# Optimization experiments

Hardware: AMD Instinct MI355X
Metric: run time of the kernel (lower is better)

The kernel has to match this reference:

```python
import jax, jax.numpy as jnp
import numpy as np

EPS = 1e-12  # torch F.normalize eps


def _l2norm(x):
    n = jnp.linalg.norm(x, axis=-1, keepdims=True)
    return x / jnp.maximum(n, EPS)


def setup_inputs() -> dict:
    key = jax.random.key(0)
    k1, k2 = jax.random.split(key)
    B, Lq, Lk, D = 128, 32, 128, 128
    left_emb = jax.random.normal(k1, (B, Lq, D), dtype=jnp.float32)
    right_emb = jax.random.normal(k2, (B, Lk, D), dtype=jnp.float32)
    pos_idx = jnp.arange(B, dtype=jnp.int64)
    logit_scale = jnp.asarray(np.log(1.0 / 0.07), dtype=jnp.float32)  # scalar param
    return {"left_emb": left_emb, "right_emb": right_emb,
            "logit_scale": logit_scale, "pos_idx": pos_idx}


def reference(left_emb, right_emb, logit_scale, pos_idx):
    # maxsim_colbert: normalize token embeddings, cross-sim, max over doc
    # tokens, sum over query tokens -> [B, B] logits, then CE loss.
    l = _l2norm(left_emb)   # [B, Lq, D]
    r = _l2norm(right_emb)  # [B, Lk, D]
    sims = jnp.einsum('xik,yjk->xyij', l, r)        # [B, B, Lq, Lk]
    sim = sims.max(axis=-1).sum(axis=-1)            # [B, B]
    logits = jnp.exp(logit_scale) * sim
    logp = jax.nn.log_softmax(logits, axis=1)
    B = logits.shape[0]
    loss = -jnp.mean(logp[jnp.arange(B), pos_idx])
    return loss
```

## Files before the change

kernel.cpp:

```cpp
#include <hip/hip_runtime.h>
#include <hip/hip_bf16.h>

typedef short bf16x8 __attribute__((ext_vector_type(8)));
typedef float f32x4 __attribute__((ext_vector_type(4)));
typedef unsigned short u16;

#define B 128
#define LQ 32
#define LK 128
#define D 128
#define YPB 4
#define TILE_BYTES 32768


static __device__ inline u16 f2bf_rne(float f) {
  union { float f; unsigned u; } v; v.f = f;
  unsigned r = v.u + 0x7fffu + ((v.u >> 16) & 1u);
  return (u16)(r >> 16);
}

__global__ __launch_bounds__(256) void normalize_kernel(
    const float* __restrict__ left, const float* __restrict__ right,
    u16* __restrict__ l_out, u16* __restrict__ r_out) {
  int wave = (blockIdx.x * blockDim.x + threadIdx.x) >> 6;
  int lane = threadIdx.x & 63;
  const int n_l = B * LQ;
  const float* src; u16* dst; int row;
  if (wave < n_l) { src = left;  dst = l_out; row = wave; }
  else            { src = right; dst = r_out; row = wave - n_l; }
  float2 v = *reinterpret_cast<const float2*>(src + (size_t)row * D + lane * 2);
  float ss = v.x * v.x + v.y * v.y;
#pragma unroll
  for (int off = 1; off < 64; off <<= 1) ss += __shfl_xor(ss, off);
  float inv = 1.0f / fmaxf(sqrtf(ss), 1e-12f);
  unsigned packed = (unsigned)f2bf_rne(v.x * inv) |
                    ((unsigned)f2bf_rne(v.y * inv) << 16);
  *reinterpret_cast<unsigned*>(dst + (size_t)row * D + lane * 2) = packed;
}

__global__ __launch_bounds__(256, 2) void maxsim_kernel(
    const u16* __restrict__ lb, const u16* __restrict__ rb,
    float* __restrict__ sims) {
  __shared__ char smem[2 * TILE_BYTES];
  const int tid  = threadIdx.x;
  const int lane = tid & 63;
  const int wv   = tid >> 6;
  const int xg   = blockIdx.x >> 5;
  const int yg   = blockIdx.x & 31;
  const int x0   = xg * 8 + wv * 2;
  const int lo4  = lane & 15, hi2 = lane >> 4;
  const int frag_off = lo4 * D + hi2 * 8;

  {
    const char* ryb = (const char*)(rb + (size_t)(yg * YPB) * LK * D);
#pragma unroll
    for (int i = 0; i < 8; ++i) {
      unsigned Lrel = (unsigned)(i * 4096 + wv * 1024 + lane * 16);
      unsigned Goff = Lrel ^ (((Lrel >> 8) & 7) << 4);
      __builtin_amdgcn_global_load_lds(
          (const __attribute__((address_space(1))) void*)(ryb + Goff),
          (__attribute__((address_space(3))) void*)(smem + i * 4096 + wv * 1024),
          16, 0, 0);
    }
  }
  bf16x8 bfr[2][2][4];
  const u16* lxbase = lb + (size_t)x0 * LQ * D;
#pragma unroll
  for (int xi = 0; xi < 2; ++xi)
#pragma unroll
    for (int ni = 0; ni < 2; ++ni)
#pragma unroll
      for (int k = 0; k < 4; ++k)
        bfr[xi][ni][k] = *reinterpret_cast<const bf16x8*>(
            lxbase + (size_t)(xi * LQ + ni * 16) * D + k * 32 + frag_off);

  for (int yy = 0; yy < YPB; ++yy) {
    if (yy + 1 < YPB) {
      const char* ryb = (const char*)(rb + (size_t)(yg * YPB + yy + 1) * LK * D);
      char* bufn = smem + ((yy + 1) & 1) * TILE_BYTES;
#pragma unroll
      for (int i = 0; i < 8; ++i) {
        unsigned Lrel = (unsigned)(i * 4096 + wv * 1024 + lane * 16);
        unsigned Goff = Lrel ^ (((Lrel >> 8) & 7) << 4);
        __builtin_amdgcn_global_load_lds(
            (const __attribute__((address_space(1))) void*)(ryb + Goff),
            (__attribute__((address_space(3))) void*)(bufn + i * 4096 + wv * 1024),
            16, 0, 0);
      }
      asm volatile("s_waitcnt vmcnt(8)" ::: "memory");
    } else {
      asm volatile("s_waitcnt vmcnt(0)" ::: "memory");
    }
    asm volatile("s_barrier" ::: "memory");

    const char* buf = smem + (yy & 1) * TILE_BYTES;
    float cmax[2][2];
#pragma unroll
    for (int xi = 0; xi < 2; ++xi)
#pragma unroll
      for (int ni = 0; ni < 2; ++ni) cmax[xi][ni] = -3.0e38f;

#pragma unroll 2
    for (int mj = 0; mj < 8; ++mj) {
      bf16x8 afr[4];
#pragma unroll
      for (int k = 0; k < 4; ++k) {
        unsigned Erel = (unsigned)((mj * 16 + lo4) * 256 + k * 64 + hi2 * 16);
        unsigned addr = Erel ^ (((Erel >> 8) & 7) << 4);
        afr[k] = *reinterpret_cast<const bf16x8*>(buf + addr);
      }
      f32x4 acc[2][2];
#pragma unroll
      for (int xi = 0; xi < 2; ++xi)
#pragma unroll
        for (int ni = 0; ni < 2; ++ni) acc[xi][ni] = f32x4{0.f, 0.f, 0.f, 0.f};
#pragma unroll
      for (int k = 0; k < 4; ++k)
#pragma unroll
        for (int xi = 0; xi < 2; ++xi)
#pragma unroll
          for (int ni = 0; ni < 2; ++ni)
            acc[xi][ni] = __builtin_amdgcn_mfma_f32_16x16x32_bf16(
                afr[k], bfr[xi][ni][k], acc[xi][ni], 0, 0, 0);
#pragma unroll
      for (int xi = 0; xi < 2; ++xi)
#pragma unroll
        for (int ni = 0; ni < 2; ++ni)
#pragma unroll
          for (int r = 0; r < 4; ++r)
            cmax[xi][ni] = fmaxf(cmax[xi][ni], acc[xi][ni][r]);
    }
    asm volatile("s_barrier" ::: "memory");

    const int y = yg * YPB + yy;
#pragma unroll
    for (int xi = 0; xi < 2; ++xi) {
      float c0 = cmax[xi][0], c1 = cmax[xi][1];
      c0 = fmaxf(c0, __shfl_xor(c0, 16)); c0 = fmaxf(c0, __shfl_xor(c0, 32));
      c1 = fmaxf(c1, __shfl_xor(c1, 16)); c1 = fmaxf(c1, __shfl_xor(c1, 32));
      float s = c0 + c1;
#pragma unroll
      for (int off = 1; off <= 8; off <<= 1) s += __shfl_xor(s, off);
      if (lane == 0) sims[(x0 + xi) * B + y] = s;
    }
  }
}

__global__ __launch_bounds__(1024) void loss_kernel(
    const float* __restrict__ sims, const float* __restrict__ logit_scale,
    const int* __restrict__ pos_idx, float* __restrict__ out) {
  __shared__ float red[16];
  const int lane = threadIdx.x & 63;
  const int wv   = threadIdx.x >> 6;
  const float scale = expf(logit_scale[0]);
  float local = 0.f;
#pragma unroll
  for (int rr = 0; rr < 8; ++rr) {
    const int x = wv * 8 + rr;
    const float* row = sims + x * B;
    float a = row[lane], b2 = row[64 + lane];
    float m = fmaxf(a, b2);
#pragma unroll
    for (int off = 1; off < 64; off <<= 1) m = fmaxf(m, __shfl_xor(m, off));
    float ml = scale * m;
    float e = expf(scale * a - ml) + expf(scale * b2 - ml);
#pragma unroll
    for (int off = 1; off < 64; off <<= 1) e += __shfl_xor(e, off);
    int pos = pos_idx[x];
    float pv = __shfl(pos < 64 ? a : b2, pos & 63);
    local += -(scale * pv - ml - logf(e));
  }
  if (lane == 0) red[wv] = local;
  __syncthreads();
  if (threadIdx.x == 0) {
    float t = 0.f;
#pragma unroll
    for (int i = 0; i < 16; ++i) t += red[i];
    out[0] = t / (float)B;
  }
}

extern "C" void kernel_launch(void* const* d_in, const int* in_sizes, int n_in,
                              void* d_out, int out_size, void* d_ws, size_t ws_size,
                              hipStream_t stream) {
  const float* left  = (const float*)d_in[0];
  const float* right = (const float*)d_in[1];
  const float* ls    = (const float*)d_in[2];
  const int*   pos   = (const int*)d_in[3];
  float* out = (float*)d_out;

  char* ws = (char*)d_ws;
  u16* lb   = (u16*)ws;
  u16* rbuf = (u16*)(ws + (size_t)B * LQ * D * 2);
  float* sims = (float*)(ws + (size_t)B * LQ * D * 2 + (size_t)B * LK * D * 2);

  int waves = B * LQ + B * LK;
  normalize_kernel<<<waves / 4, 256, 0, stream>>>(left, right, lb, rbuf);
  maxsim_kernel<<<512, 256, 0, stream>>>(lb, rbuf, sims);
  loss_kernel<<<1, 1024, 0, stream>>>(sims, ls, pos, out);
}
```

Measured before the change: 35.47 us.

## Switch maxsim to 32x32x16 MFMA with wider LDS swizzle and full unroll

Replaces the 16x16x32 bf16 MFMA tiling with 32x32x16 MFMA so each wave covers all 32 query tokens per instruction, changing fragment layouts, LDS addressing and the max/sum reduction accordingly. The LDS XOR swizzle is widened to 16 chunks to match the new read pattern and avoid bank conflicts, and per-lane base addresses are precomputed. The y-loop is fully unrolled and s_setprio is raised around the MFMA chain. This aims to cut MFMA instruction count and LDS read overhead, at the cost of larger accumulators and higher register pressure.

```diff
diff --git a/kernel.cpp b/kernel.cpp
--- a/kernel.cpp
+++ b/kernel.cpp
@@ -2,7 +2,7 @@
 #include <hip/hip_bf16.h>
 
 typedef short bf16x8 __attribute__((ext_vector_type(8)));
-typedef float f32x4 __attribute__((ext_vector_type(4)));
+typedef float f32x16 __attribute__((ext_vector_type(16)));
 typedef unsigned short u16;
 
 #define B 128
@@ -17,6 +17,10 @@
   union { float f; unsigned u; } v; v.f = f;
   unsigned r = v.u + 0x7fffu + ((v.u >> 16) & 1u);
   return (u16)(r >> 16);
+}
+
+static __device__ inline unsigned swz(unsigned a) {
+  return a ^ (((a >> 8) & 15u) << 4);
 }
 
 __global__ __launch_bounds__(256) void normalize_kernel(
@@ -48,32 +52,41 @@
   const int xg   = blockIdx.x >> 5;
   const int yg   = blockIdx.x & 31;
   const int x0   = xg * 8 + wv * 2;
-  const int lo4  = lane & 15, hi2 = lane >> 4;
-  const int frag_off = lo4 * D + hi2 * 8;
+  const unsigned rr = lane & 31;
+  const unsigned hh = (unsigned)lane >> 5;
 
   {
     const char* ryb = (const char*)(rb + (size_t)(yg * YPB) * LK * D);
 #pragma unroll
     for (int i = 0; i < 8; ++i) {
       unsigned Lrel = (unsigned)(i * 4096 + wv * 1024 + lane * 16);
-      unsigned Goff = Lrel ^ (((Lrel >> 8) & 7) << 4);
       __builtin_amdgcn_global_load_lds(
-          (const __attribute__((address_space(1))) void*)(ryb + Goff),
+          (const __attribute__((address_space(1))) void*)(ryb + swz(Lrel)),
           (__attribute__((address_space(3))) void*)(smem + i * 4096 + wv * 1024),
           16, 0, 0);
     }
   }
-  bf16x8 bfr[2][2][4];
-  const u16* lxbase = lb + (size_t)x0 * LQ * D;
-#pragma unroll
-  for (int xi = 0; xi < 2; ++xi)
-#pragma unroll
-    for (int ni = 0; ni < 2; ++ni)
-#pragma unroll
-      for (int k = 0; k < 4; ++k)
-        bfr[xi][ni][k] = *reinterpret_cast<const bf16x8*>(
-            lxbase + (size_t)(xi * LQ + ni * 16) * D + k * 32 + frag_off);
-
+
+  unsigned kbase[8];
+  const unsigned msk = rr & 15u;
+#pragma unroll
+  for (int ks = 0; ks < 8; ++ks)
+    kbase[ks] = rr * 256u + (((((unsigned)ks << 1) | hh) ^ msk) << 4);
+
+  bf16x8 bfr[2][8];
+#pragma unroll
+  for (int xi = 0; xi < 2; ++xi) {
+    const u16* lx = lb + (size_t)(x0 + xi) * LQ * D + (size_t)rr * D;
+#pragma unroll
+    for (int ks = 0; ks < 8; ++ks)
+      bfr[xi][ks] = *reinterpret_cast<const bf16x8*>(lx + ks * 16 + hh * 8);
+  }
+
+  f32x16 z;
+#pragma unroll
+  for (int t = 0; t < 16; ++t) z[t] = 0.f;
+
+#pragma unroll
   for (int yy = 0; yy < YPB; ++yy) {
     if (yy + 1 < YPB) {
       const char* ryb = (const char*)(rb + (size_t)(yg * YPB + yy + 1) * LK * D);
@@ -81,9 +94,8 @@
 #pragma unroll
       for (int i = 0; i < 8; ++i) {
         unsigned Lrel = (unsigned)(i * 4096 + wv * 1024 + lane * 16);
-        unsigned Goff = Lrel ^ (((Lrel >> 8) & 7) << 4);
         __builtin_amdgcn_global_load_lds(
-            (const __attribute__((address_space(1))) void*)(ryb + Goff),
+            (const __attribute__((address_space(1))) void*)(ryb + swz(Lrel)),
             (__attribute__((address_space(3))) void*)(bufn + i * 4096 + wv * 1024),
             16, 0, 0);
       }
@@ -94,54 +106,45 @@
     asm volatile("s_barrier" ::: "memory");
 
     const char* buf = smem + (yy & 1) * TILE_BYTES;
-    float cmax[2][2];
-#pragma unroll
-    for (int xi = 0; xi < 2; ++xi)
-#pragma unroll
-      for (int ni = 0; ni < 2; ++ni) cmax[xi][ni] = -3.0e38f;
-
-#pragma unroll 2
-    for (int mj = 0; mj < 8; ++mj) {
-      bf16x8 afr[4];
-#pragma unroll
-      for (int k = 0; k < 4; ++k) {
-        unsigned Erel = (unsigned)((mj * 16 + lo4) * 256 + k * 64 + hi2 * 16);
-        unsigned addr = Erel ^ (((Erel >> 8) & 7) << 4);
-        afr[k] = *reinterpret_cast<const bf16x8*>(buf + addr);
+    float cm0 = -3.0e38f, cm1 = -3.0e38f;
+
+#pragma unroll
+    for (int mj = 0; mj < 4; ++mj) {
+      bf16x8 afr[8];
+#pragma unroll
+      for (int ks = 0; ks < 8; ++ks)
+        afr[ks] = *reinterpret_cast<const bf16x8*>(buf + mj * 8192 + kbase[ks]);
+      __builtin_amdgcn_s_setprio(1);
+      f32x16 a0 = __builtin_amdgcn_mfma_f32_32x32x16_bf16(afr[0], bfr[0][0], z, 0, 0, 0);
+      f32x16 a1 = __builtin_amdgcn_mfma_f32_32x32x16_bf16(afr[0], bfr[1][0], z, 0, 0, 0);
+#pragma unroll
+      for (int ks = 1; ks < 8; ++ks) {
+        a0 = __builtin_amdgcn_mfma_f32_32x32x16_bf16(afr[ks], bfr[0][ks], a0, 0, 0, 0);
+        a1 = __builtin_amdgcn_mfma_f32_32x32x16_bf16(afr[ks], bfr[1][ks], a1, 0, 0, 0);
       }
-      f32x4 acc[2][2];
-#pragma unroll
-      for (int xi = 0; xi < 2; ++xi)
-#pragma unroll
-        for (int ni = 0; ni < 2; ++ni) acc[xi][ni] = f32x4{0.f, 0.f, 0.f, 0.f};
-#pragma unroll
-      for (int k = 0; k < 4; ++k)
-#pragma unroll
-        for (int xi = 0; xi < 2; ++xi)
-#pragma unroll
-          for (int ni = 0; ni < 2; ++ni)
-            acc[xi][ni] = __builtin_amdgcn_mfma_f32_16x16x32_bf16(
-                afr[k], bfr[xi][ni][k], acc[xi][ni], 0, 0, 0);
-#pragma unroll
-      for (int xi = 0; xi < 2; ++xi)
-#pragma unroll
-        for (int ni = 0; ni < 2; ++ni)
-#pragma unroll
-          for (int r = 0; r < 4; ++r)
-            cmax[xi][ni] = fmaxf(cmax[xi][ni], acc[xi][ni][r]);
+      __builtin_amdgcn_s_setprio(0);
+      float t0, t1;
+#pragma unroll
+      for (int t = 0; t < 16; t += 4) {
+        t0 = fmaxf(fmaxf(a0[t], a0[t + 1]), fmaxf(a0[t + 2], a0[t + 3]));
+        t1 = fmaxf(fmaxf(a1[t], a1[t + 1]), fmaxf(a1[t + 2], a1[t + 3]));
+        cm0 = fmaxf(cm0, t0);
+        cm1 = fmaxf(cm1, t1);
+      }
     }
     asm volatile("s_barrier" ::: "memory");
 
     const int y = yg * YPB + yy;
-#pragma unroll
-    for (int xi = 0; xi < 2; ++xi) {
-      float c0 = cmax[xi][0], c1 = cmax[xi][1];
-      c0 = fmaxf(c0, __shfl_xor(c0, 16)); c0 = fmaxf(c0, __shfl_xor(c0, 32));
-      c1 = fmaxf(c1, __shfl_xor(c1, 16)); c1 = fmaxf(c1, __shfl_xor(c1, 32));
-      float s = c0 + c1;
-#pragma unroll
-      for (int off = 1; off <= 8; off <<= 1) s += __shfl_xor(s, off);
-      if (lane == 0) sims[(x0 + xi) * B + y] = s;
+    cm0 = fmaxf(cm0, __shfl_xor(cm0, 32));
+    cm1 = fmaxf(cm1, __shfl_xor(cm1, 32));
+#pragma unroll
+    for (int off = 1; off <= 16; off <<= 1) {
+      cm0 += __shfl_xor(cm0, off);
+      cm1 += __shfl_xor(cm1, off);
+    }
+    if (lane == 0) {
+      sims[(x0 + 0) * B + y] = cm0;
+      sims[(x0 + 1) * B + y] = cm1;
     }
   }
 }
```

New measurement: 34.78 us. About the same (-1.9%).
